# Kernel optimization log

Measured on AMD Instinct MI355X. Metric: run time of the kernel, lower is better.

Reference implementation:

```python
import jax, jax.numpy as jnp
import numpy as np

B, S, IN, HID, NH, HD, R, WIN, TK = 2, 2048, 64, 512, 8, 64, 64, 5, 16
C1, C2, C3 = 171, 171, 170  # hidden_dim split across 3 conv branches (512 = 171+171+170)


def _conv(xc, w, b, pad):
    y = jax.lax.conv_general_dilated(xc, w, window_strides=(1,), padding=[(pad, pad)],
                                     dimension_numbers=('NCH', 'OIH', 'NCH'))
    return jax.nn.relu(y + b[None, :, None])


def setup_inputs():
    key = jax.random.key(0)
    ks = jax.random.split(key, 22)
    p = lambda k, sh: jax.random.normal(k, sh, jnp.float32) * 0.05
    return {
        'x': jax.random.normal(ks[0], (B, S, IN), jnp.float32),
        'conv1_w': p(ks[1], (C1, IN, 3)), 'conv1_b': p(ks[2], (C1,)),
        'conv2_w': p(ks[3], (C2, IN, 5)), 'conv2_b': p(ks[4], (C2,)),
        'conv3_w': p(ks[5], (C3, IN, 7)), 'conv3_b': p(ks[6], (C3,)),
        'Wq': p(ks[7], (HID, HID)), 'bq': p(ks[8], (HID,)),
        'Wk': p(ks[9], (HID, HID)), 'bk': p(ks[10], (HID,)),
        'Wv': p(ks[11], (HID, HID)), 'bv': p(ks[12], (HID,)),
        'Wkp': p(ks[13], (R, HD)), 'bkp': p(ks[14], (R,)),
        'Wvp': p(ks[15], (R, HD)), 'bvp': p(ks[16], (R,)),
        'Wo': p(ks[17], (HID, HID)), 'bo': p(ks[18], (HID,)),
        'ln_g': jnp.ones((HID,), jnp.float32), 'ln_b': jnp.zeros((HID,), jnp.float32),
    }


def reference(x, conv1_w, conv1_b, conv2_w, conv2_b, conv3_w, conv3_b,
              Wq, bq, Wk, bk, Wv, bv, Wkp, bkp, Wvp, bvp, Wo, bo, ln_g, ln_b):
    # multi-scale conv front-end
    xc = x.transpose(0, 2, 1)  # [B, IN, S]
    h = jnp.concatenate([_conv(xc, conv1_w, conv1_b, 1),
                         _conv(xc, conv2_w, conv2_b, 2),
                         _conv(xc, conv3_w, conv3_b, 3)], axis=1).transpose(0, 2, 1)  # [B,S,HID]

    def heads(W_, b_):
        return (h @ W_.T + b_).reshape(B, S, NH, HD).transpose(0, 2, 1, 3)  # [B,NH,S,HD]

    Q, K, V = heads(Wq, bq), heads(Wk, bk), heads(Wv, bv)
    Kp = K @ Wkp.T + bkp  # [B,NH,S,R]
    Vp = V @ Wvp.T + bvp

    # local sliding-window attention; -inf masking reproduces the per-t boundary slicing
    hw = WIN // 2
    idx = jnp.arange(S)[:, None] + jnp.arange(-hw, hw + 1)[None, :]
    valid = (idx >= 0) & (idx < S)
    idxc = jnp.clip(idx, 0, S - 1)
    Kw = K[:, :, idxc, :]
    Vw = V[:, :, idxc, :]
    ls = jnp.einsum('bhsd,bhswd->bhsw', Q, Kw) / jnp.sqrt(jnp.float32(HD))
    ls = jnp.where(valid[None, None], ls, -jnp.inf)
    local = jnp.einsum('bhsw,bhswd->bhsd', jax.nn.softmax(ls, axis=-1), Vw)

    # top-k low-rank global attention (HD == R required by original einsum)
    gs = jnp.einsum('bhqd,bhkd->bhqk', Q, Kp) / jnp.sqrt(jnp.float32(R))  # [B,NH,S,S]
    tv, ti = jax.lax.top_k(gs, TK)
    tw = jax.nn.softmax(tv, axis=-1)  # [B,NH,S,TK]
    bi = jnp.arange(B)[:, None, None, None]
    hi = jnp.arange(NH)[None, :, None, None]
    topV = Vp[bi, hi, ti]  # [B,NH,S,TK,R]
    sp = jnp.einsum('bhqk,bhqkr->bhqr', tw, topV)
    sp = sp @ Wvp.T + bvp  # extra value_proj applied to sparse output, as in original

    out = ((local + sp) * 0.5).transpose(0, 2, 1, 3).reshape(B, S, HID)
    out = out @ Wo.T + bo
    res = out + h
    mu = res.mean(-1, keepdims=True)
    var = ((res - mu) ** 2).mean(-1, keepdims=True)
    return (res - mu) / jnp.sqrt(var + 1e-5) * ln_g + ln_b
```

## Files before the change

### kernel.cpp

```cpp
#include <hip/hip_runtime.h>
#include <hip/hip_bf16.h>

#define BB 2
#define SS 2048
#define INC 64
#define HIDN 512
#define NHH 8
#define HDD 64
#define SP 2054

typedef __attribute__((ext_vector_type(8))) short bf16x8;
typedef __attribute__((ext_vector_type(4))) float f32x4;

__device__ __forceinline__ short f2bf(float f) {
  union { __hip_bfloat16 h; short s; } u;
  u.h = __float2bfloat16(f);
  return u.s;
}
__device__ __forceinline__ float bf2f(short s) {
  return __uint_as_float(((unsigned)(unsigned short)s) << 16);
}


__global__ __launch_bounds__(256) void prep_kernel(
    const float* __restrict__ x, const float* __restrict__ w1,
    const float* __restrict__ b1, const float* __restrict__ w2,
    const float* __restrict__ b2, const float* __restrict__ w3,
    const float* __restrict__ b3, const float* __restrict__ Wq,
    const float* __restrict__ Wk_, const float* __restrict__ Wv_,
    const float* __restrict__ bq, const float* __restrict__ bk_,
    const float* __restrict__ bv_, const float* __restrict__ Wo,
    const float* __restrict__ Wkp, const float* __restrict__ Wvp,
    const float* __restrict__ bvp, short* __restrict__ Wallbf,
    float* __restrict__ ball, short* __restrict__ Wobf,
    short* __restrict__ Wkpbf, short* __restrict__ W2bf,
    float* __restrict__ cvec, short* __restrict__ xbfp,
    short* __restrict__ Wcbf, float* __restrict__ bcat) {
  int i0 = blockIdx.x * 256 + threadIdx.x;
  int stride = gridDim.x * 256;
  for (int g = i0; g < 98304; g += stride) {
    int n = g >> 6;
    int k = (g & 63) << 3;
    const float* src;
    if (n < 512)       src = Wq  + (size_t)n * 512 + k;
    else if (n < 1024) src = Wk_ + (size_t)(n - 512) * 512 + k;
    else               src = Wv_ + (size_t)(n - 1024) * 512 + k;
    float4 f0 = *(const float4*)src;
    float4 f1 = *(const float4*)(src + 4);
    bf16x8 v;
    v[0] = f2bf(f0.x); v[1] = f2bf(f0.y); v[2] = f2bf(f0.z); v[3] = f2bf(f0.w);
    v[4] = f2bf(f1.x); v[5] = f2bf(f1.y); v[6] = f2bf(f1.z); v[7] = f2bf(f1.w);
    size_t off = (size_t)(n >> 6) * 32768 + (size_t)(k >> 5) * 2048 +
                 (size_t)((n & 63) >> 4) * 512 +
                 ((((k & 31) >> 3) * 16 + (n & 15)) << 3);
    *(bf16x8*)(Wallbf + off) = v;
  }
  for (int g = i0; g < 32768; g += stride) {
    int n = g >> 6;
    int k = (g & 63) << 3;
    const float* src = Wo + (size_t)n * 512 + k;
    float4 f0 = *(const float4*)src;
    float4 f1 = *(const float4*)(src + 4);
    bf16x8 v;
    v[0] = f2bf(f0.x); v[1] = f2bf(f0.y); v[2] = f2bf(f0.z); v[3] = f2bf(f0.w);
    v[4] = f2bf(f1.x); v[5] = f2bf(f1.y); v[6] = f2bf(f1.z); v[7] = f2bf(f1.w);
    size_t off = (size_t)(n >> 6) * 32768 + (size_t)(k >> 5) * 2048 +
                 (size_t)((n & 63) >> 4) * 512 +
                 ((((k & 31) >> 3) * 16 + (n & 15)) << 3);
    *(bf16x8*)(Wobf + off) = v;
  }
  for (int g = i0; g < BB * SP * 8; g += stride) {
    int row = g >> 3, c0 = (g & 7) << 3;
    int b = row / SP, pr = row - b * SP;
    int sg = pr - 3;
    bf16x8 v;
    if (sg >= 0 && sg < SS) {
      const float* src = x + ((size_t)(b * SS + sg) << 6) + c0;
      float4 f0 = *(const float4*)src;
      float4 f1 = *(const float4*)(src + 4);
      v[0] = f2bf(f0.x); v[1] = f2bf(f0.y); v[2] = f2bf(f0.z); v[3] = f2bf(f0.w);
      v[4] = f2bf(f1.x); v[5] = f2bf(f1.y); v[6] = f2bf(f1.z); v[7] = f2bf(f1.w);
    } else {
#pragma unroll
      for (int e = 0; e < 8; e++) v[e] = 0;
    }
    *(bf16x8*)(xbfp + ((size_t)row << 6) + c0) = v;
  }
  for (int g = i0; g < 28672; g += stride) {
    int c = g / 56;
    int rem = g - c * 56;
    int k = rem << 3;
    int t = k >> 6;
    int ci0 = k & 63;
    bf16x8 v;
#pragma unroll
    for (int e = 0; e < 8; e++) {
      int ci = ci0 + e;
      float val = 0.f;
      if (c < 171) {
        int kk = t - 2;
        if (kk >= 0 && kk < 3) val = w1[(c * 64 + ci) * 3 + kk];
      } else if (c < 342) {
        int kk = t - 1;
        if (kk >= 0 && kk < 5) val = w2[((c - 171) * 64 + ci) * 5 + kk];
      } else {
        val = w3[((c - 342) * 64 + ci) * 7 + t];
      }
      v[e] = f2bf(val);
    }
    size_t off = (size_t)(c >> 6) * 28672 + (size_t)(k >> 5) * 2048 +
                 (size_t)((c & 63) >> 4) * 512 +
                 ((((k & 31) >> 3) * 16 + (c & 15)) << 3);
    *(bf16x8*)(Wcbf + off) = v;
  }
  for (int idx = i0; idx < 4096; idx += stride) {
    Wkpbf[idx] = f2bf(Wkp[idx]);
    int j = idx >> 6, d = idx & 63;
    float s = 0.f;
#pragma unroll 8
    for (int i = 0; i < 64; i++) s += Wvp[j * 64 + i] * Wvp[i * 64 + d];
    W2bf[idx] = f2bf(s);
  }
  if (i0 < 1536) {
    float v;
    if (i0 < 512)       v = bq[i0];
    else if (i0 < 1024) v = bk_[i0 - 512];
    else                v = bv_[i0 - 1024];
    ball[i0] = v;
  }
  if (i0 < 512) {
    float v;
    if (i0 < 171)      v = b1[i0];
    else if (i0 < 342) v = b2[i0 - 171];
    else               v = b3[i0 - 342];
    bcat[i0] = v;
  }
  if (i0 < 64) {
    float s = bvp[i0];
#pragma unroll 8
    for (int i = 0; i < 64; i++) s += bvp[i] * Wvp[i0 * 64 + i];
    cvec[i0] = s;
  }
}

__global__ __launch_bounds__(256, 4) void gemm_conv(
    const short* __restrict__ xbfp, const short* __restrict__ Wcbf,
    const float* __restrict__ bcat, short* __restrict__ hbf,
    short* __restrict__ hAf) {
  int m0 = blockIdx.x * 128;
  int n0 = blockIdx.y * 64;
  int tid = threadIdx.x;
  int wvv = tid >> 6, lane = tid & 63;
  int quad = lane >> 4, l16 = lane & 15;
  int mw = m0 + wvv * 32;
  int r0 = mw + l16, r1 = r0 + 16;
  int b0 = r0 >> 11, s0 = r0 & 2047;
  int b1 = r1 >> 11, s1 = r1 & 2047;
  const short* ap0 = xbfp + (size_t)(b0 * SP + s0) * 64 + quad * 8;
  const short* ap1 = xbfp + (size_t)(b1 * SP + s1) * 64 + quad * 8;
  const short* bp = Wcbf + (size_t)(n0 >> 6) * 28672 + lane * 8;
  f32x4 acc[2][4] = {};
  bf16x8 cA0 = *(const bf16x8*)ap0;
  bf16x8 cA1 = *(const bf16x8*)ap1;
  bf16x8 cB0 = *(const bf16x8*)(bp + 0 * 512);
  bf16x8 cB1 = *(const bf16x8*)(bp + 1 * 512);
  bf16x8 cB2 = *(const bf16x8*)(bp + 2 * 512);
  bf16x8 cB3 = *(const bf16x8*)(bp + 3 * 512);
#pragma unroll 2
  for (int ks = 0; ks < 14; ks++) {
    int kn = (ks + 1 < 14 ? ks + 1 : 13);
    int offa = kn * 32;
    int offb = kn * 2048;
    bf16x8 nA0 = *(const bf16x8*)(ap0 + offa);
    bf16x8 nA1 = *(const bf16x8*)(ap1 + offa);
    bf16x8 nB0 = *(const bf16x8*)(bp + offb + 0 * 512);
    bf16x8 nB1 = *(const bf16x8*)(bp + offb + 1 * 512);
    bf16x8 nB2 = *(const bf16x8*)(bp + offb + 2 * 512);
    bf16x8 nB3 = *(const bf16x8*)(bp + offb + 3 * 512);
    acc[0][0] = __builtin_amdgcn_mfma_f32_16x16x32_bf16(cA0, cB0, acc[0][0], 0, 0, 0);
    acc[1][0] = __builtin_amdgcn_mfma_f32_16x16x32_bf16(cA1, cB0, acc[1][0], 0, 0, 0);
    acc[0][1] = __builtin_amdgcn_mfma_f32_16x16x32_bf16(cA0, cB1, acc[0][1], 0, 0, 0);
    acc[1][1] = __builtin_amdgcn_mfma_f32_16x16x32_bf16(cA1, cB1, acc[1][1], 0, 0, 0);
    acc[0][2] = __builtin_amdgcn_mfma_f32_16x16x32_bf16(cA0, cB2, acc[0][2], 0, 0, 0);
    acc[1][2] = __builtin_amdgcn_mfma_f32_16x16x32_bf16(cA1, cB2, acc[1][2], 0, 0, 0);
    acc[0][3] = __builtin_amdgcn_mfma_f32_16x16x32_bf16(cA0, cB3, acc[0][3], 0, 0, 0);
    acc[1][3] = __builtin_amdgcn_mfma_f32_16x16x32_bf16(cA1, cB3, acc[1][3], 0, 0, 0);
    cA0 = nA0; cA1 = nA1;
    cB0 = nB0; cB1 = nB1; cB2 = nB2; cB3 = nB3;
  }
#pragma unroll
  for (int mt = 0; mt < 2; mt++) {
#pragma unroll
    for (int r = 0; r < 4; r++) {
      int m = mw + mt * 16 + quad * 4 + r;
      size_t abase = (size_t)(m >> 4) * 8192;
      int m15 = m & 15;
#pragma unroll
      for (int t = 0; t < 4; t++) {
        int n = n0 + t * 16 + l16;
        float v = fmaxf(acc[mt][t][r] + bcat[n], 0.f);
        short val = f2bf(v);
        hbf[(size_t)m * 512 + n] = val;
        hAf[abase + (size_t)(n >> 5) * 512 +
            ((((n & 31) >> 3) * 16 + m15) << 3) + (n & 7)] = val;
      }
    }
  }
}

__global__ __launch_bounds__(256, 4) void gemm_qkv(
    const short* __restrict__ hAf, const short* __restrict__ Wbf,
    const float* __restrict__ bias, short* __restrict__ Qh,
    short* __restrict__ Kh, short* __restrict__ Vh) {
  int m0 = blockIdx.x * 128;
  int n0 = blockIdx.y * 64;
  int tid = threadIdx.x;
  int wvv = tid >> 6, lane = tid & 63;
  int quad = lane >> 4, l16 = lane & 15;
  int mw = m0 + wvv * 32;
  const short* ap0 = hAf + (size_t)(mw >> 4) * 8192 + lane * 8;
  const short* ap1 = ap0 + 8192;
  const short* bp = Wbf + (size_t)(n0 >> 6) * 32768 + lane * 8;
  f32x4 acc[2][4] = {};
  bf16x8 cA0 = *(const bf16x8*)ap0;
  bf16x8 cA1 = *(const bf16x8*)ap1;
  bf16x8 cB0 = *(const bf16x8*)(bp + 0 * 512);
  bf16x8 cB1 = *(const bf16x8*)(bp + 1 * 512);
  bf16x8 cB2 = *(const bf16x8*)(bp + 2 * 512);
  bf16x8 cB3 = *(const bf16x8*)(bp + 3 * 512);
#pragma unroll 2
  for (int ks = 0; ks < 16; ks++) {
    int kn = (ks + 1 < 16 ? ks + 1 : 15);
    int offab = kn * 512;
    int offb = kn * 2048;
    bf16x8 nA0 = *(const bf16x8*)(ap0 + offab);
    bf16x8 nA1 = *(const bf16x8*)(ap1 + offab);
    bf16x8 nB0 = *(const bf16x8*)(bp + offb + 0 * 512);
    bf16x8 nB1 = *(const bf16x8*)(bp + offb + 1 * 512);
    bf16x8 nB2 = *(const bf16x8*)(bp + offb + 2 * 512);
    bf16x8 nB3 = *(const bf16x8*)(bp + offb + 3 * 512);
    acc[0][0] = __builtin_amdgcn_mfma_f32_16x16x32_bf16(cA0, cB0, acc[0][0], 0, 0, 0);
    acc[1][0] = __builtin_amdgcn_mfma_f32_16x16x32_bf16(cA1, cB0, acc[1][0], 0, 0, 0);
    acc[0][1] = __builtin_amdgcn_mfma_f32_16x16x32_bf16(cA0, cB1, acc[0][1], 0, 0, 0);
    acc[1][1] = __builtin_amdgcn_mfma_f32_16x16x32_bf16(cA1, cB1, acc[1][1], 0, 0, 0);
    acc[0][2] = __builtin_amdgcn_mfma_f32_16x16x32_bf16(cA0, cB2, acc[0][2], 0, 0, 0);
    acc[1][2] = __builtin_amdgcn_mfma_f32_16x16x32_bf16(cA1, cB2, acc[1][2], 0, 0, 0);
    acc[0][3] = __builtin_amdgcn_mfma_f32_16x16x32_bf16(cA0, cB3, acc[0][3], 0, 0, 0);
    acc[1][3] = __builtin_amdgcn_mfma_f32_16x16x32_bf16(cA1, cB3, acc[1][3], 0, 0, 0);
    cA0 = nA0; cA1 = nA1;
    cB0 = nB0; cB1 = nB1; cB2 = nB2; cB3 = nB3;
  }
  int which = n0 >> 9;
  int head = (n0 >> 6) & 7;
  short* dst = which == 0 ? Qh : (which == 1 ? Kh : Vh);
  float scale = which == 0 ? 0.125f : 1.0f;
#pragma unroll
  for (int mt = 0; mt < 2; mt++) {
#pragma unroll
    for (int r = 0; r < 4; r++) {
      int m = mw + mt * 16 + quad * 4 + r;
      int bb = m >> 11, s = m & 2047;
      size_t rowoff = ((size_t)(bb * 8 + head) * 2048 + s) * 64;
#pragma unroll
      for (int t = 0; t < 4; t++) {
        int hd = t * 16 + l16;
        float v = acc[mt][t][r] + bias[n0 + hd];
        dst[rowoff + hd] = f2bf(v * scale);
      }
    }
  }
}

__global__ __launch_bounds__(256, 4) void kpvp_local_kernel(
    const short* __restrict__ Kh, const short* __restrict__ Vh,
    const short* __restrict__ Wkpbf, const float* __restrict__ bkp,
    const short* __restrict__ W2bf, const float* __restrict__ cvec,
    short* __restrict__ Kfrag, float* __restrict__ Vpp,
    const short* __restrict__ Qh, float* __restrict__ ctxl) {
  int tid = threadIdx.x;
  __shared__ float Sloc[4][2][16][17];
  __shared__ float wloc[4][16][8];
  if (blockIdx.x < 256) {
    int m0 = blockIdx.x * 128;
    int wvv = tid >> 6, lane = tid & 63;
    int quad = lane >> 4, l16 = lane & 15;
    int mw = m0 + wvv * 32;
    {
      const short* ap0 = Kh + (size_t)(mw + l16) * 64 + quad * 8;
      const short* ap1 = ap0 + 16 * 64;
      const short* bp = Wkpbf + l16 * 64 + quad * 8;
      bf16x8 A00 = *(const bf16x8*)ap0, A01 = *(const bf16x8*)(ap0 + 32);
      bf16x8 A10 = *(const bf16x8*)ap1, A11 = *(const bf16x8*)(ap1 + 32);
      f32x4 acc[2][4] = {};
#pragma unroll
      for (int t = 0; t < 4; t++) {
        bf16x8 B0 = *(const bf16x8*)(bp + t * 16 * 64);
        bf16x8 B1 = *(const bf16x8*)(bp + t * 16 * 64 + 32);
        acc[0][t] = __builtin_amdgcn_mfma_f32_16x16x32_bf16(A00, B0, acc[0][t], 0, 0, 0);
        acc[0][t] = __builtin_amdgcn_mfma_f32_16x16x32_bf16(A01, B1, acc[0][t], 0, 0, 0);
        acc[1][t] = __builtin_amdgcn_mfma_f32_16x16x32_bf16(A10, B0, acc[1][t], 0, 0, 0);
        acc[1][t] = __builtin_amdgcn_mfma_f32_16x16x32_bf16(A11, B1, acc[1][t], 0, 0, 0);
      }
#pragma unroll
      for (int mt = 0; mt < 2; mt++)
#pragma unroll
        for (int r = 0; r < 4; r++) {
          int m = mw + mt * 16 + quad * 4 + r;
          int m15 = m & 15;
          size_t gbase = (size_t)(m >> 4) * 1024;
#pragma unroll
          for (int t = 0; t < 4; t++) {
            int n = t * 16 + l16;
            short val = f2bf(acc[mt][t][r] + bkp[n]);
            Kfrag[gbase + (size_t)(n >> 5) * 512 +
                  ((((n & 31) >> 3) * 16 + m15) << 3) + (n & 7)] = val;
          }
        }
    }
    {
      const short* ap0 = Vh + (size_t)(mw + l16) * 64 + quad * 8;
      const short* ap1 = ap0 + 16 * 64;
      const short* bp = W2bf + l16 * 64 + quad * 8;
      bf16x8 A00 = *(const bf16x8*)ap0, A01 = *(const bf16x8*)(ap0 + 32);
      bf16x8 A10 = *(const bf16x8*)ap1, A11 = *(const bf16x8*)(ap1 + 32);
      f32x4 acc[2][4] = {};
#pragma unroll
      for (int t = 0; t < 4; t++) {
        bf16x8 B0 = *(const bf16x8*)(bp + t * 16 * 64);
        bf16x8 B1 = *(const bf16x8*)(bp + t * 16 * 64 + 32);
        acc[0][t] = __builtin_amdgcn_mfma_f32_16x16x32_bf16(A00, B0, acc[0][t], 0, 0, 0);
        acc[0][t] = __builtin_amdgcn_mfma_f32_16x16x32_bf16(A01, B1, acc[0][t], 0, 0, 0);
        acc[1][t] = __builtin_amdgcn_mfma_f32_16x16x32_bf16(A10, B0, acc[1][t], 0, 0, 0);
        acc[1][t] = __builtin_amdgcn_mfma_f32_16x16x32_bf16(A11, B1, acc[1][t], 0, 0, 0);
      }
#pragma unroll
      for (int mt = 0; mt < 2; mt++)
#pragma unroll
        for (int r = 0; r < 4; r++) {
          int m = mw + mt * 16 + quad * 4 + r;
#pragma unroll
          for (int t = 0; t < 4; t++) {
            int n = t * 16 + l16;
            Vpp[(size_t)m * 64 + n] = acc[mt][t][r] + cvec[n];
          }
        }
    }
    return;
  }
  int wv = tid >> 6;
  int tile = (blockIdx.x - 256) * 4 + wv;
  int bh = tile >> 7;
  int q0 = (tile & 127) * 16;
  int lane = tid & 63;
  int quad = lane >> 4, l16 = lane & 15;

  const short* qbase = Qh + (size_t)(bh * 2048 + q0 + l16) * 64 + quad * 8;
  bf16x8 a0 = *(const bf16x8*)qbase;
  bf16x8 a1 = *(const bf16x8*)(qbase + 32);

  int k0a = min(max(q0 - 2 + l16, 0), 2047);
  int k1a = min(q0 + 6 + l16, 2047);
  const short* kb0 = Kh + (size_t)(bh * 2048 + k0a) * 64 + quad * 8;
  const short* kb1 = Kh + (size_t)(bh * 2048 + k1a) * 64 + quad * 8;
  bf16x8 B00 = *(const bf16x8*)kb0;
  bf16x8 B01 = *(const bf16x8*)(kb0 + 32);
  bf16x8 B10 = *(const bf16x8*)kb1;
  bf16x8 B11 = *(const bf16x8*)(kb1 + 32);
  f32x4 C0 = {0.f, 0.f, 0.f, 0.f};
  f32x4 C1 = {0.f, 0.f, 0.f, 0.f};
  C0 = __builtin_amdgcn_mfma_f32_16x16x32_bf16(a0, B00, C0, 0, 0, 0);
  C0 = __builtin_amdgcn_mfma_f32_16x16x32_bf16(a1, B01, C0, 0, 0, 0);
  C1 = __builtin_amdgcn_mfma_f32_16x16x32_bf16(a0, B10, C1, 0, 0, 0);
  C1 = __builtin_amdgcn_mfma_f32_16x16x32_bf16(a1, B11, C1, 0, 0, 0);
#pragma unroll
  for (int r = 0; r < 4; r++) {
    Sloc[wv][0][quad * 4 + r][l16] = C0[r];
    Sloc[wv][1][quad * 4 + r][l16] = C1[r];
  }
  __builtin_amdgcn_wave_barrier();
  if (lane < 16) {
    int q = lane;
    float sc[5];
    bool ok[5];
#pragma unroll
    for (int j = 0; j < 5; j++) {
      int offq = q + j - 2;
      int sg = q0 + offq;
      ok[j] = (sg >= 0 && sg < SS);
      int t = offq <= 13 ? 0 : 1;
      int col = t ? offq - 6 : offq + 2;
      sc[j] = ok[j] ? Sloc[wv][t][q][col] : -3.0e38f;
    }
    float m = -3.0e38f;
#pragma unroll
    for (int j = 0; j < 5; j++) m = fmaxf(m, sc[j]);
    float e[5], l = 0.f;
#pragma unroll
    for (int j = 0; j < 5; j++) {
      e[j] = ok[j] ? __expf(sc[j] - m) : 0.f;
      l += e[j];
    }
    float inv = 1.f / l;
#pragma unroll
    for (int j = 0; j < 5; j++) wloc[wv][q][j] = e[j] * inv;
  }
  __builtin_amdgcn_wave_barrier();
  {
    int q = lane >> 2, jb = (lane & 3) * 16;
    int s = q0 + q;
    float acc[16] = {};
#pragma unroll
    for (int j = 0; j < 5; j++) {
      int sg = s + j - 2;
      if (sg >= 0 && sg < SS) {
        float w = wloc[wv][q][j];
        const short* vr = Vh + (size_t)(bh * 2048 + sg) * 64 + jb;
#pragma unroll
        for (int u = 0; u < 16; u += 4) {
          short4 v4 = *(const short4*)(vr + u);
          acc[u + 0] += w * bf2f(v4.x);
          acc[u + 1] += w * bf2f(v4.y);
          acc[u + 2] += w * bf2f(v4.z);
          acc[u + 3] += w * bf2f(v4.w);
        }
      }
    }
    float* orow = ctxl + (size_t)(bh * 2048 + s) * 64 + jb;
#pragma unroll
    for (int u = 0; u < 16; u += 4)
      *(float4*)(orow + u) =
          make_float4(acc[u], acc[u + 1], acc[u + 2], acc[u + 3]);
  }
}

__global__ __launch_bounds__(256, 4) void global_attn(
    const short* __restrict__ Qh, const short* __restrict__ Kfrag,
    const float* __restrict__ Vpp, const float* __restrict__ ctxl,
    short* __restrict__ ctxcb) {
  int tid = threadIdx.x;
  int wv = tid >> 6;
  int lane = tid & 63;
  int quad = lane >> 4, l16 = lane & 15;
  int tb = wv >> 1;
  int half = wv & 1;
  int p = blockIdx.x;
  int bh = (p & 7) * 2 + ((p >> 3) & 1);
  int seg = p >> 4;
  int tile = seg * 2 + tb;
  int q0 = tile * 16;

  __shared__ unsigned swl[4][16][17];
  __shared__ float twl[2][16][17];
  __shared__ int   txl[2][16][17];

  const short* qbase = Qh + (size_t)(bh * 2048 + q0 + l16) * 64 + quad * 8;
  bf16x8 a0 = *(const bf16x8*)qbase;
  bf16x8 a1 = *(const bf16x8*)(qbase + 32);

  const short* kf =
      Kfrag + (size_t)bh * (128 * 1024) + (size_t)half * (64 * 1024) + lane * 8;

  unsigned er[4][8];
#pragma unroll
  for (int a = 0; a < 4; a++)
#pragma unroll
    for (int j = 0; j < 8; j++) er[a][j] = 0u;

  auto insert8 = [&](unsigned (&e)[8], unsigned cand) {
    unsigned n0, n1, n2, n3, n4, n5, n6, n7;
    asm("v_max_u32 %0, %1, %2" : "=v"(n0) : "v"(e[0]), "v"(cand));
    asm("v_med3_u32 %0, %1, %2, %3" : "=v"(n1) : "v"(e[0]), "v"(e[1]), "v"(cand));
    asm("v_med3_u32 %0, %1, %2, %3" : "=v"(n2) : "v"(e[1]), "v"(e[2]), "v"(cand));
    asm("v_med3_u32 %0, %1, %2, %3" : "=v"(n3) : "v"(e[2]), "v"(e[3]), "v"(cand));
    asm("v_med3_u32 %0, %1, %2, %3" : "=v"(n4) : "v"(e[3]), "v"(e[4]), "v"(cand));
    asm("v_med3_u32 %0, %1, %2, %3" : "=v"(n5) : "v"(e[4]), "v"(e[5]), "v"(cand));
    asm("v_med3_u32 %0, %1, %2, %3" : "=v"(n6) : "v"(e[5]), "v"(e[6]), "v"(cand));
    asm("v_med3_u32 %0, %1, %2, %3" : "=v"(n7) : "v"(e[6]), "v"(e[7]), "v"(cand));
    e[0] = n0; e[1] = n1; e[2] = n2; e[3] = n3;
    e[4] = n4; e[5] = n5; e[6] = n6; e[7] = n7;
  };
  auto mkcand = [&](float s, int idxr) -> unsigned {
    unsigned u = __float_as_uint(s);
    u ^= ((unsigned)((int)u >> 31)) | 0x80000000u;
    return (u & 0xFFFFF800u) | (unsigned)idxr;
  };

  int idxb = 2047 - half * 1024 - l16;
#pragma unroll 4
  for (int g = 0; g < 64; g++) {
    bf16x8 B00 = *(const bf16x8*)(kf + g * 1024);
    bf16x8 B01 = *(const bf16x8*)(kf + g * 1024 + 512);
    f32x4 C0 = {0.f, 0.f, 0.f, 0.f};
    C0 = __builtin_amdgcn_mfma_f32_16x16x32_bf16(a0, B00, C0, 0, 0, 0);
    C0 = __builtin_amdgcn_mfma_f32_16x16x32_bf16(a1, B01, C0, 0, 0, 0);
    int idxr = idxb - (g << 4);
    insert8(er[0], mkcand(C0[0], idxr));
    insert8(er[1], mkcand(C0[1], idxr));
    insert8(er[2], mkcand(C0[2], idxr));
    insert8(er[3], mkcand(C0[3], idxr));
  }

  {
    unsigned sw[4] = {0u, 0u, 0u, 0u};
#pragma unroll
    for (int t = 0; t < 16; t++) {
#pragma unroll
      for (int a = 0; a < 4; a++) {
        unsigned w = er[a][0];
#pragma unroll
        for (int mm = 1; mm <= 8; mm <<= 1) {
          unsigned o = (unsigned)__shfl_xor((int)w, mm);
          w = w > o ? w : o;
        }
        bool pop = (er[a][0] == w);
#pragma unroll
        for (int j = 0; j < 7; j++) er[a][j] = pop ? er[a][j + 1] : er[a][j];
        er[a][7] = pop ? 0u : er[a][7];
        if (l16 == t) sw[a] = w;
      }
    }
#pragma unroll
    for (int a = 0; a < 4; a++) swl[wv][quad * 4 + a][l16] = sw[a];
  }
  __syncthreads();

  if (tid < 32) {
    int tb2 = tid >> 4, q = tid & 15;
    const unsigned* A = swl[tb2 * 2][q];
    const unsigned* Bv = swl[tb2 * 2 + 1][q];
    auto decode = [&](unsigned w) -> float {
      unsigned wb = w & 0xFFFFF800u;
      unsigned uu = (w & 0x80000000u) ? (wb ^ 0x80000000u) : ~wb;
      return (w == 0u) ? -1.0e30f : __uint_as_float(uu);
    };
    unsigned h0 = A[0], h1 = Bv[0];
    float mval = decode(h0 > h1 ? h0 : h1);
    float lsum = 0.f;
    float ev[16];
    int ki[16];
#pragma unroll
    for (int i = 0; i < 16; i++) {
      unsigned wa = A[i], wb2 = Bv[15 - i];
      unsigned w = wa > wb2 ? wa : wb2;
      float sv = decode(w);
      float ex = __expf(sv - mval);
      lsum += ex;
      ev[i] = ex;
      ki[i] = 2047 - (int)(w & 0x7FFu);
    }
    float inv = 1.f / lsum;
#pragma unroll
    for (int i = 0; i < 16; i++) {
      twl[tb2][q][i] = ev[i] * inv;
      txl[tb2][q][i] = ki[i];
    }
  }
  __syncthreads();

  {
    int tb2 = tid >> 7;
    int r = tid & 127;
    int q = r >> 3, d0 = (r & 7) * 8;
    int tile2 = seg * 2 + tb2;
    int q02 = tile2 * 16;
    int b = bh >> 3, hh = bh & 7;
    const float* vball = Vpp + (size_t)bh * (2048 * 64) + d0;
    float acc[8];
#pragma unroll
    for (int u = 0; u < 8; u++) acc[u] = 0.f;
#pragma unroll 4
    for (int j = 0; j < 16; j++) {
      float w = twl[tb2][q][j];
      const float* vr = vball + (size_t)txl[tb2][q][j] * 64;
      float4 v0 = *(const float4*)vr;
      float4 v1 = *(const float4*)(vr + 4);
      acc[0] += w * v0.x; acc[1] += w * v0.y;
      acc[2] += w * v0.z; acc[3] += w * v0.w;
      acc[4] += w * v1.x; acc[5] += w * v1.y;
      acc[6] += w * v1.z; acc[7] += w * v1.w;
    }
    int s = q02 + q;
    const float* lrow = ctxl + (size_t)(bh * 2048 + s) * 64 + d0;
    int M = b * 2048 + s;
    int k = hh * 64 + d0;
    size_t aoff = (size_t)(M >> 4) * 8192 + (size_t)(k >> 5) * 512 +
                  ((((k & 31) >> 3) * 16 + (M & 15)) << 3);
    float4 lv0 = *(const float4*)lrow;
    float4 lv1 = *(const float4*)(lrow + 4);
    short4 o0, o1;
    o0.x = f2bf(0.5f * (lv0.x + acc[0]));
    o0.y = f2bf(0.5f * (lv0.y + acc[1]));
    o0.z = f2bf(0.5f * (lv0.z + acc[2]));
    o0.w = f2bf(0.5f * (lv0.w + acc[3]));
    o1.x = f2bf(0.5f * (lv1.x + acc[4]));
    o1.y = f2bf(0.5f * (lv1.y + acc[5]));
    o1.z = f2bf(0.5f * (lv1.z + acc[6]));
    o1.w = f2bf(0.5f * (lv1.w + acc[7]));
    *(short4*)(ctxcb + aoff) = o0;
    *(short4*)(ctxcb + aoff + 4) = o1;
  }
}

__global__ __launch_bounds__(256, 4) void gemm_wo(
    const short* __restrict__ Abf, const short* __restrict__ Wbf,
    const float* __restrict__ bo, const short* __restrict__ hbf,
    float* __restrict__ outp) {
  int m0 = blockIdx.x * 128;
  int n0 = blockIdx.y * 64;
  int tid = threadIdx.x;
  int wvv = tid >> 6, lane = tid & 63;
  int quad = lane >> 4, l16 = lane & 15;
  int mw = m0 + wvv * 32;
  const short* ap0 = Abf + (size_t)(mw >> 4) * 8192 + lane * 8;
  const short* ap1 = ap0 + 8192;
  const short* bp = Wbf + (size_t)(n0 >> 6) * 32768 + lane * 8;
  f32x4 acc[2][4] = {};
  bf16x8 cA0 = *(const bf16x8*)ap0;
  bf16x8 cA1 = *(const bf16x8*)ap1;
  bf16x8 cB0 = *(const bf16x8*)(bp + 0 * 512);
  bf16x8 cB1 = *(const bf16x8*)(bp + 1 * 512);
  bf16x8 cB2 = *(const bf16x8*)(bp + 2 * 512);
  bf16x8 cB3 = *(const bf16x8*)(bp + 3 * 512);
#pragma unroll 2
  for (int ks = 0; ks < 16; ks++) {
    int kn = (ks + 1 < 16 ? ks + 1 : 15);
    int offab = kn * 512;
    int offb = kn * 2048;
    bf16x8 nA0 = *(const bf16x8*)(ap0 + offab);
    bf16x8 nA1 = *(const bf16x8*)(ap1 + offab);
    bf16x8 nB0 = *(const bf16x8*)(bp + offb + 0 * 512);
    bf16x8 nB1 = *(const bf16x8*)(bp + offb + 1 * 512);
    bf16x8 nB2 = *(const bf16x8*)(bp + offb + 2 * 512);
    bf16x8 nB3 = *(const bf16x8*)(bp + offb + 3 * 512);
    acc[0][0] = __builtin_amdgcn_mfma_f32_16x16x32_bf16(cA0, cB0, acc[0][0], 0, 0, 0);
    acc[1][0] = __builtin_amdgcn_mfma_f32_16x16x32_bf16(cA1, cB0, acc[1][0], 0, 0, 0);
    acc[0][1] = __builtin_amdgcn_mfma_f32_16x16x32_bf16(cA0, cB1, acc[0][1], 0, 0, 0);
    acc[1][1] = __builtin_amdgcn_mfma_f32_16x16x32_bf16(cA1, cB1, acc[1][1], 0, 0, 0);
    acc[0][2] = __builtin_amdgcn_mfma_f32_16x16x32_bf16(cA0, cB2, acc[0][2], 0, 0, 0);
    acc[1][2] = __builtin_amdgcn_mfma_f32_16x16x32_bf16(cA1, cB2, acc[1][2], 0, 0, 0);
    acc[0][3] = __builtin_amdgcn_mfma_f32_16x16x32_bf16(cA0, cB3, acc[0][3], 0, 0, 0);
    acc[1][3] = __builtin_amdgcn_mfma_f32_16x16x32_bf16(cA1, cB3, acc[1][3], 0, 0, 0);
    cA0 = nA0; cA1 = nA1;
    cB0 = nB0; cB1 = nB1; cB2 = nB2; cB3 = nB3;
  }
#pragma unroll
  for (int mt = 0; mt < 2; mt++) {
#pragma unroll
    for (int r = 0; r < 4; r++) {
      int m = mw + mt * 16 + quad * 4 + r;
#pragma unroll
      for (int t = 0; t < 4; t++) {
        int n = n0 + t * 16 + l16;
        outp[(size_t)m * 512 + n] =
            acc[mt][t][r] + bo[n] + bf2f(hbf[(size_t)m * 512 + n]);
      }
    }
  }
}

__global__ __launch_bounds__(256) void ln_kernel(float* __restrict__ o,
                                                 const float* __restrict__ g,
                                                 const float* __restrict__ bb) {
  int row = blockIdx.x;
  int tid = threadIdx.x;
  float v0 = o[row * 512 + tid];
  float v1 = o[row * 512 + 256 + tid];
  float s = v0 + v1;
  float s2 = v0 * v0 + v1 * v1;
#pragma unroll
  for (int off = 1; off < 64; off <<= 1) {
    s += __shfl_xor(s, off);
    s2 += __shfl_xor(s2, off);
  }
  __shared__ float ps[4], ps2[4];
  int w = tid >> 6;
  if ((tid & 63) == 0) { ps[w] = s; ps2[w] = s2; }
  __syncthreads();
  float S = ps[0] + ps[1] + ps[2] + ps[3];
  float S2 = ps2[0] + ps2[1] + ps2[2] + ps2[3];
  float mu = S * (1.f / 512.f);
  float var = S2 * (1.f / 512.f) - mu * mu;
  float inv = rsqrtf(var + 1e-5f);
  o[row * 512 + tid] = (v0 - mu) * inv * g[tid] + bb[tid];
  o[row * 512 + 256 + tid] = (v1 - mu) * inv * g[tid + 256] + bb[tid + 256];
}

extern "C" void kernel_launch(void* const* d_in, const int* in_sizes, int n_in,
                              void* d_out, int out_size, void* d_ws,
                              size_t ws_size, hipStream_t stream) {
  const float* x   = (const float*)d_in[0];
  const float* w1  = (const float*)d_in[1];
  const float* b1  = (const float*)d_in[2];
  const float* w2  = (const float*)d_in[3];
  const float* b2  = (const float*)d_in[4];
  const float* w3  = (const float*)d_in[5];
  const float* b3  = (const float*)d_in[6];
  const float* Wq  = (const float*)d_in[7];
  const float* bq  = (const float*)d_in[8];
  const float* Wk  = (const float*)d_in[9];
  const float* bk  = (const float*)d_in[10];
  const float* Wv  = (const float*)d_in[11];
  const float* bv  = (const float*)d_in[12];
  const float* Wkp = (const float*)d_in[13];
  const float* bkp = (const float*)d_in[14];
  const float* Wvp = (const float*)d_in[15];
  const float* bvp = (const float*)d_in[16];
  const float* Wo  = (const float*)d_in[17];
  const float* bo  = (const float*)d_in[18];
  const float* lng = (const float*)d_in[19];
  const float* lnb = (const float*)d_in[20];

  float* p = (float*)d_ws;
  short* Wallbf = (short*)p;  p += 786432;
  float* ball   = p;          p += 2048;
  short* Wobf   = (short*)p;  p += 262144;
  short* Wkpbf  = (short*)p;  p += 4096;
  short* W2bf   = (short*)p;  p += 4096;
  float* cvec   = p;          p += 64;
  short* xbfp   = (short*)p;  p += 262912;
  short* Wcbf   = (short*)p;  p += 229376;
  float* bcat   = p;          p += 512;
  short* hbf    = (short*)p;  p += 1048576;
  short* hAf    = (short*)p;  p += 1048576;
  short* Qh     = (short*)p;  p += 1048576;
  short* Kh     = (short*)p;  p += 1048576;
  short* Vh     = (short*)p;  p += 1048576;
  short* Kfrag  = (short*)p;  p += 1048576;
  float* Vpp    = p;          p += 2097152;
  float* ctxl   = p;          p += 2097152;
  short* ctxcb  = (short*)p;  p += 1048576;
  float* outF   = (float*)d_out;

  prep_kernel<<<512, 256, 0, stream>>>(x, w1, b1, w2, b2, w3, b3, Wq, Wk, Wv,
                                       bq, bk, bv, Wo, Wkp, Wvp, bvp, Wallbf,
                                       ball, Wobf, Wkpbf, W2bf, cvec, xbfp,
                                       Wcbf, bcat);
  {
    dim3 g(32, 8);
    gemm_conv<<<g, 256, 0, stream>>>(xbfp, Wcbf, bcat, hbf, hAf);
  }
  {
    dim3 g(32, 24);
    gemm_qkv<<<g, 256, 0, stream>>>(hAf, Wallbf, ball, Qh, Kh, Vh);
  }
  kpvp_local_kernel<<<768, 256, 0, stream>>>(Kh, Vh, Wkpbf, bkp, W2bf, cvec,
                                             Kfrag, Vpp, Qh, ctxl);
  global_attn<<<1024, 256, 0, stream>>>(Qh, Kfrag, Vpp, ctxl, ctxcb);
  {
    dim3 g(32, 8);
    gemm_wo<<<g, 256, 0, stream>>>(ctxcb, Wobf, bo, hbf, outF);
  }
  ln_kernel<<<4096, 256, 0, stream>>>(outF, lng, lnb);
}
```

Baseline: 222.5 us.

## Fuse LayerNorm into Wo GEMM and move weight casts into conv GEMM

Moves the bf16 conversion of Wq/Wk/Wv/Wo out of the prep kernel into extra blocks of the conv GEMM launch, so the weight casts run alongside the conv work. It also rewrites the Wo GEMM so each 512-thread block computes a full 16-row by 512-column tile, stages it in shared memory, and applies LayerNorm in place. This removes the separate LN kernel and the fp32 write and re-read of the output. The cost is a smaller M tile per block with less A reuse, 256 large blocks, and a roughly 33 KB shared buffer that limits occupancy.

Result: faster. 210.7 us (median of 2 runs) (-5.3%).

```diff
diff --git a/kernel.cpp b/kernel.cpp
--- a/kernel.cpp
+++ b/kernel.cpp
@@ -26,49 +26,15 @@
     const float* __restrict__ x, const float* __restrict__ w1,
     const float* __restrict__ b1, const float* __restrict__ w2,
     const float* __restrict__ b2, const float* __restrict__ w3,
-    const float* __restrict__ b3, const float* __restrict__ Wq,
-    const float* __restrict__ Wk_, const float* __restrict__ Wv_,
-    const float* __restrict__ bq, const float* __restrict__ bk_,
-    const float* __restrict__ bv_, const float* __restrict__ Wo,
+    const float* __restrict__ b3, const float* __restrict__ bq,
+    const float* __restrict__ bk_, const float* __restrict__ bv_,
     const float* __restrict__ Wkp, const float* __restrict__ Wvp,
-    const float* __restrict__ bvp, short* __restrict__ Wallbf,
-    float* __restrict__ ball, short* __restrict__ Wobf,
+    const float* __restrict__ bvp, float* __restrict__ ball,
     short* __restrict__ Wkpbf, short* __restrict__ W2bf,
     float* __restrict__ cvec, short* __restrict__ xbfp,
     short* __restrict__ Wcbf, float* __restrict__ bcat) {
   int i0 = blockIdx.x * 256 + threadIdx.x;
   int stride = gridDim.x * 256;
-  for (int g = i0; g < 98304; g += stride) {
-    int n = g >> 6;
-    int k = (g & 63) << 3;
-    const float* src;
-    if (n < 512)       src = Wq  + (size_t)n * 512 + k;
-    else if (n < 1024) src = Wk_ + (size_t)(n - 512) * 512 + k;
-    else               src = Wv_ + (size_t)(n - 1024) * 512 + k;
-    float4 f0 = *(const float4*)src;
-    float4 f1 = *(const float4*)(src + 4);
-    bf16x8 v;
-    v[0] = f2bf(f0.x); v[1] = f2bf(f0.y); v[2] = f2bf(f0.z); v[3] = f2bf(f0.w);
-    v[4] = f2bf(f1.x); v[5] = f2bf(f1.y); v[6] = f2bf(f1.z); v[7] = f2bf(f1.w);
-    size_t off = (size_t)(n >> 6) * 32768 + (size_t)(k >> 5) * 2048 +
-                 (size_t)((n & 63) >> 4) * 512 +
-                 ((((k & 31) >> 3) * 16 + (n & 15)) << 3);
-    *(bf16x8*)(Wallbf + off) = v;
-  }
-  for (int g = i0; g < 32768; g += stride) {
-    int n = g >> 6;
-    int k = (g & 63) << 3;
-    const float* src = Wo + (size_t)n * 512 + k;
-    float4 f0 = *(const float4*)src;
-    float4 f1 = *(const float4*)(src + 4);
-    bf16x8 v;
-    v[0] = f2bf(f0.x); v[1] = f2bf(f0.y); v[2] = f2bf(f0.z); v[3] = f2bf(f0.w);
-    v[4] = f2bf(f1.x); v[5] = f2bf(f1.y); v[6] = f2bf(f1.z); v[7] = f2bf(f1.w);
-    size_t off = (size_t)(n >> 6) * 32768 + (size_t)(k >> 5) * 2048 +
-                 (size_t)((n & 63) >> 4) * 512 +
-                 ((((k & 31) >> 3) * 16 + (n & 15)) << 3);
-    *(bf16x8*)(Wobf + off) = v;
-  }
   for (int g = i0; g < BB * SP * 8; g += stride) {
     int row = g >> 3, c0 = (g & 7) << 3;
     int b = row / SP, pr = row - b * SP;
@@ -143,13 +109,52 @@
   }
 }
 
-__global__ __launch_bounds__(256, 4) void gemm_conv(
+__global__ __launch_bounds__(256, 4) void gemm_conv_fused(
     const short* __restrict__ xbfp, const short* __restrict__ Wcbf,
     const float* __restrict__ bcat, short* __restrict__ hbf,
-    short* __restrict__ hAf) {
-  int m0 = blockIdx.x * 128;
-  int n0 = blockIdx.y * 64;
+    short* __restrict__ hAf, const float* __restrict__ Wq,
+    const float* __restrict__ Wk_, const float* __restrict__ Wv_,
+    const float* __restrict__ Wo, short* __restrict__ Wallbf,
+    short* __restrict__ Wobf) {
+  int blk = blockIdx.x;
   int tid = threadIdx.x;
+  if (blk >= 256) {
+    int i0 = (blk - 256) * 256 + tid;
+    if (i0 < 98304) {
+      int n = i0 >> 6;
+      int k = (i0 & 63) << 3;
+      const float* src;
+      if (n < 512)       src = Wq  + (size_t)n * 512 + k;
+      else if (n < 1024) src = Wk_ + (size_t)(n - 512) * 512 + k;
+      else               src = Wv_ + (size_t)(n - 1024) * 512 + k;
+      float4 f0 = *(const float4*)src;
+      float4 f1 = *(const float4*)(src + 4);
+      bf16x8 v;
+      v[0] = f2bf(f0.x); v[1] = f2bf(f0.y); v[2] = f2bf(f0.z); v[3] = f2bf(f0.w);
+      v[4] = f2bf(f1.x); v[5] = f2bf(f1.y); v[6] = f2bf(f1.z); v[7] = f2bf(f1.w);
+      size_t off = (size_t)(n >> 6) * 32768 + (size_t)(k >> 5) * 2048 +
+                   (size_t)((n & 63) >> 4) * 512 +
+                   ((((k & 31) >> 3) * 16 + (n & 15)) << 3);
+      *(bf16x8*)(Wallbf + off) = v;
+    } else {
+      int g = i0 - 98304;
+      int n = g >> 6;
+      int k = (g & 63) << 3;
+      const float* src = Wo + (size_t)n * 512 + k;
+      float4 f0 = *(const float4*)src;
+      float4 f1 = *(const float4*)(src + 4);
+      bf16x8 v;
+      v[0] = f2bf(f0.x); v[1] = f2bf(f0.y); v[2] = f2bf(f0.z); v[3] = f2bf(f0.w);
+      v[4] = f2bf(f1.x); v[5] = f2bf(f1.y); v[6] = f2bf(f1.z); v[7] = f2bf(f1.w);
+      size_t off = (size_t)(n >> 6) * 32768 + (size_t)(k >> 5) * 2048 +
+                   (size_t)((n & 63) >> 4) * 512 +
+                   ((((k & 31) >> 3) * 16 + (n & 15)) << 3);
+      *(bf16x8*)(Wobf + off) = v;
+    }
+    return;
+  }
+  int m0 = (blk >> 3) * 128;
+  int n0 = (blk & 7) * 64;
   int wvv = tid >> 6, lane = tid & 63;
   int quad = lane >> 4, l16 = lane & 15;
   int mw = m0 + wvv * 32;
@@ -601,22 +606,25 @@
   }
 }
 
-__global__ __launch_bounds__(256, 4) void gemm_wo(
+__global__ __launch_bounds__(512, 2) void gemm_wo_ln(
     const short* __restrict__ Abf, const short* __restrict__ Wbf,
     const float* __restrict__ bo, const short* __restrict__ hbf,
+    const float* __restrict__ g, const float* __restrict__ bb,
     float* __restrict__ outp) {
-  int m0 = blockIdx.x * 128;
-  int n0 = blockIdx.y * 64;
+  int blk = blockIdx.x;
+  int m0 = blk * 16;
   int tid = threadIdx.x;
   int wvv = tid >> 6, lane = tid & 63;
   int quad = lane >> 4, l16 = lane & 15;
-  int mw = m0 + wvv * 32;
-  const short* ap0 = Abf + (size_t)(mw >> 4) * 8192 + lane * 8;
-  const short* ap1 = ap0 + 8192;
-  const short* bp = Wbf + (size_t)(n0 >> 6) * 32768 + lane * 8;
-  f32x4 acc[2][4] = {};
-  bf16x8 cA0 = *(const bf16x8*)ap0;
-  bf16x8 cA1 = *(const bf16x8*)ap1;
+  int n0 = wvv * 64;
+
+  __shared__ float rowbuf[16][516];
+  __shared__ float mus[16], invs[16];
+
+  const short* ap = Abf + (size_t)blk * 8192 + lane * 8;
+  const short* bp = Wbf + (size_t)wvv * 32768 + lane * 8;
+  f32x4 acc[4] = {};
+  bf16x8 cA = *(const bf16x8*)ap;
   bf16x8 cB0 = *(const bf16x8*)(bp + 0 * 512);
   bf16x8 cB1 = *(const bf16x8*)(bp + 1 * 512);
   bf16x8 cB2 = *(const bf16x8*)(bp + 2 * 512);
@@ -624,65 +632,66 @@
 #pragma unroll 2
   for (int ks = 0; ks < 16; ks++) {
     int kn = (ks + 1 < 16 ? ks + 1 : 15);
-    int offab = kn * 512;
-    int offb = kn * 2048;
-    bf16x8 nA0 = *(const bf16x8*)(ap0 + offab);
-    bf16x8 nA1 = *(const bf16x8*)(ap1 + offab);
-    bf16x8 nB0 = *(const bf16x8*)(bp + offb + 0 * 512);
-    bf16x8 nB1 = *(const bf16x8*)(bp + offb + 1 * 512);
-    bf16x8 nB2 = *(const bf16x8*)(bp + offb + 2 * 512);
-    bf16x8 nB3 = *(const bf16x8*)(bp + offb + 3 * 512);
-    acc[0][0] = __builtin_amdgcn_mfma_f32_16x16x32_bf16(cA0, cB0, acc[0][0], 0, 0, 0);
-    acc[1][0] = __builtin_amdgcn_mfma_f32_16x16x32_bf16(cA1, cB0, acc[1][0], 0, 0, 0);
-    acc[0][1] = __builtin_amdgcn_mfma_f32_16x16x32_bf16(cA0, cB1, acc[0][1], 0, 0, 0);
-    acc[1][1] = __builtin_amdgcn_mfma_f32_16x16x32_bf16(cA1, cB1, acc[1][1], 0, 0, 0);
-    acc[0][2] = __builtin_amdgcn_mfma_f32_16x16x32_bf16(cA0, cB2, acc[0][2], 0, 0, 0);
-    acc[1][2] = __builtin_amdgcn_mfma_f32_16x16x32_bf16(cA1, cB2, acc[1][2], 0, 0, 0);
-    acc[0][3] = __builtin_amdgcn_mfma_f32_16x16x32_bf16(cA0, cB3, acc[0][3], 0, 0, 0);
-    acc[1][3] = __builtin_amdgcn_mfma_f32_16x16x32_bf16(cA1, cB3, acc[1][3], 0, 0, 0);
-    cA0 = nA0; cA1 = nA1;
+    bf16x8 nA = *(const bf16x8*)(ap + kn * 512);
+    bf16x8 nB0 = *(const bf16x8*)(bp + kn * 2048 + 0 * 512);
+    bf16x8 nB1 = *(const bf16x8*)(bp + kn * 2048 + 1 * 512);
+    bf16x8 nB2 = *(const bf16x8*)(bp + kn * 2048 + 2 * 512);
+    bf16x8 nB3 = *(const bf16x8*)(bp + kn * 2048 + 3 * 512);
+    acc[0] = __builtin_amdgcn_mfma_f32_16x16x32_bf16(cA, cB0, acc[0], 0, 0, 0);
+    acc[1] = __builtin_amdgcn_mfma_f32_16x16x32_bf16(cA, cB1, acc[1], 0, 0, 0);
+    acc[2] = __builtin_amdgcn_mfma_f32_16x16x32_bf16(cA, cB2, acc[2], 0, 0, 0);
+    acc[3] = __builtin_amdgcn_mfma_f32_16x16x32_bf16(cA, cB3, acc[3], 0, 0, 0);
+    cA = nA;
     cB0 = nB0; cB1 = nB1; cB2 = nB2; cB3 = nB3;
   }
 #pragma unroll
-  for (int mt = 0; mt < 2; mt++) {
-#pragma unroll
-    for (int r = 0; r < 4; r++) {
-      int m = mw + mt * 16 + quad * 4 + r;
-#pragma unroll
-      for (int t = 0; t < 4; t++) {
-        int n = n0 + t * 16 + l16;
-        outp[(size_t)m * 512 + n] =
-            acc[mt][t][r] + bo[n] + bf2f(hbf[(size_t)m * 512 + n]);
-      }
-    }
-  }
-}
-
-__global__ __launch_bounds__(256) void ln_kernel(float* __restrict__ o,
-                                                 const float* __restrict__ g,
-                                                 const float* __restrict__ bb) {
-  int row = blockIdx.x;
-  int tid = threadIdx.x;
-  float v0 = o[row * 512 + tid];
-  float v1 = o[row * 512 + 256 + tid];
-  float s = v0 + v1;
-  float s2 = v0 * v0 + v1 * v1;
-#pragma unroll
-  for (int off = 1; off < 64; off <<= 1) {
-    s += __shfl_xor(s, off);
-    s2 += __shfl_xor(s2, off);
-  }
-  __shared__ float ps[4], ps2[4];
-  int w = tid >> 6;
-  if ((tid & 63) == 0) { ps[w] = s; ps2[w] = s2; }
+  for (int r = 0; r < 4; r++) {
+    int rr = quad * 4 + r;
+    int m = m0 + rr;
+#pragma unroll
+    for (int t = 0; t < 4; t++) {
+      int n = n0 + t * 16 + l16;
+      rowbuf[rr][n] = acc[t][r] + bo[n] + bf2f(hbf[(size_t)m * 512 + n]);
+    }
+  }
   __syncthreads();
-  float S = ps[0] + ps[1] + ps[2] + ps[3];
-  float S2 = ps2[0] + ps2[1] + ps2[2] + ps2[3];
-  float mu = S * (1.f / 512.f);
-  float var = S2 * (1.f / 512.f) - mu * mu;
-  float inv = rsqrtf(var + 1e-5f);
-  o[row * 512 + tid] = (v0 - mu) * inv * g[tid] + bb[tid];
-  o[row * 512 + 256 + tid] = (v1 - mu) * inv * g[tid + 256] + bb[tid + 256];
+  {
+    int row = tid >> 5, seg = tid & 31;
+    float s = 0.f, s2 = 0.f;
+#pragma unroll
+    for (int u = 0; u < 16; u++) {
+      float v = rowbuf[row][seg * 16 + u];
+      s += v;
+      s2 += v * v;
+    }
+#pragma unroll
+    for (int off = 1; off < 32; off <<= 1) {
+      s += __shfl_xor(s, off);
+      s2 += __shfl_xor(s2, off);
+    }
+    if (seg == 0) {
+      float mu = s * (1.f / 512.f);
+      float var = s2 * (1.f / 512.f) - mu * mu;
+      mus[row] = mu;
+      invs[row] = rsqrtf(var + 1e-5f);
+    }
+  }
+  __syncthreads();
+  {
+    int row = tid >> 5, seg = tid & 31;
+    float mu = mus[row], inv = invs[row];
+    float* orow = outp + (size_t)(m0 + row) * 512 + seg * 16;
+#pragma unroll
+    for (int u = 0; u < 16; u += 4) {
+      int c = seg * 16 + u;
+      float4 o;
+      o.x = (rowbuf[row][c + 0] - mu) * inv * g[c + 0] + bb[c + 0];
+      o.y = (rowbuf[row][c + 1] - mu) * inv * g[c + 1] + bb[c + 1];
+      o.z = (rowbuf[row][c + 2] - mu) * inv * g[c + 2] + bb[c + 2];
+      o.w = (rowbuf[row][c + 3] - mu) * inv * g[c + 3] + bb[c + 3];
+      *(float4*)(orow + u) = o;
+    }
+  }
 }
 
 extern "C" void kernel_launch(void* const* d_in, const int* in_sizes, int n_in,
@@ -731,14 +740,11 @@
   short* ctxcb  = (short*)p;  p += 1048576;
   float* outF   = (float*)d_out;
 
-  prep_kernel<<<512, 256, 0, stream>>>(x, w1, b1, w2, b2, w3, b3, Wq, Wk, Wv,
-                                       bq, bk, bv, Wo, Wkp, Wvp, bvp, Wallbf,
-                                       ball, Wobf, Wkpbf, W2bf, cvec, xbfp,
-                                       Wcbf, bcat);
-  {
-    dim3 g(32, 8);
-    gemm_conv<<<g, 256, 0, stream>>>(xbfp, Wcbf, bcat, hbf, hAf);
-  }
+  prep_kernel<<<128, 256, 0, stream>>>(x, w1, b1, w2, b2, w3, b3, bq, bk, bv,
+                                       Wkp, Wvp, bvp, ball, Wkpbf, W2bf, cvec,
+                                       xbfp, Wcbf, bcat);
+  gemm_conv_fused<<<768, 256, 0, stream>>>(xbfp, Wcbf, bcat, hbf, hAf, Wq, Wk,
+                                           Wv, Wo, Wallbf, Wobf);
   {
     dim3 g(32, 24);
     gemm_qkv<<<g, 256, 0, stream>>>(hAf, Wallbf, ball, Qh, Kh, Vh);
@@ -746,9 +752,5 @@
   kpvp_local_kernel<<<768, 256, 0, stream>>>(Kh, Vh, Wkpbf, bkp, W2bf, cvec,
                                              Kfrag, Vpp, Qh, ctxl);
   global_attn<<<1024, 256, 0, stream>>>(Qh, Kfrag, Vpp, ctxl, ctxcb);
-  {
-    dim3 g(32, 8);
-    gemm_wo<<<g, 256, 0, stream>>>(ctxcb, Wobf, bo, hbf, outF);
-  }
-  ln_kernel<<<4096, 256, 0, stream>>>(outF, lng, lnb);
-}
+  gemm_wo_ln<<<256, 512, 0, stream>>>(ctxcb, Wobf, bo, hbf, lng, lnb, outF);
+}
```
